# Performance work log

Hardware: AMD Instinct MI355X
Metric: run time of the kernel (lower is better)

Reference implementation:

```python
import jax, jax.numpy as jnp
import numpy as np

T, B = 128, 256
C_IN, H = 1024, 1024


def setup_inputs() -> dict:
    key = jax.random.key(0)
    ks = jax.random.split(key, 6)
    x = jax.random.normal(ks[0], (T * B, C_IN), dtype=jnp.float32)
    Wi = jax.random.normal(ks[1], (C_IN, 4 * H), dtype=jnp.float32) / np.sqrt(C_IN)
    Wh = jax.random.normal(ks[2], (H, 4 * H), dtype=jnp.float32) / np.sqrt(H)
    b = jax.random.normal(ks[3], (4 * H,), dtype=jnp.float32) * 0.01
    done = jax.random.randint(ks[4], (T * B,), 0, 2) > 0
    main = jax.random.randint(ks[5], (T * B,), 0, 2) > 0
    zeros = jnp.zeros((B, H), dtype=jnp.float32)
    return {"x": x, "c1": zeros, "h1": zeros, "c2": zeros, "h2": zeros,
            "Wi": Wi, "Wh": Wh, "b": b, "done": done, "main": main}


def reference(x, c1, h1, c2, h2, Wi, Wh, b, done, main):
    batch = c1.shape[0]
    num_steps = x.shape[0] // batch
    x3 = x.reshape(num_steps, batch, -1)
    done3 = done.reshape(num_steps, batch)
    main3 = main.reshape(num_steps, batch)

    def step(carry, inp):
        (r1c, r1h), (r2c, r2h) = carry
        xt, dt, mt = inp
        m = mt[:, None]  # [B,1] select player-1 vs player-2 state
        c = jnp.where(m, r1c, r2c)
        h = jnp.where(m, r1h, r2h)
        # OptimizedLSTMCell: fused gates, flax order i, f, g, o
        z = xt @ Wi + h @ Wh + b
        i, f, g, o = jnp.split(z, 4, axis=-1)
        nc = jax.nn.sigmoid(f) * c + jax.nn.sigmoid(i) * jnp.tanh(g)
        nh = jax.nn.sigmoid(o) * jnp.tanh(nc)
        # write back only to the active player's state
        n1c = jnp.where(m, nc, r1c); n1h = jnp.where(m, nh, r1h)
        n2c = jnp.where(m, r2c, nc); n2h = jnp.where(m, r2h, nh)
        # reset both states where episode is done
        d = dt[:, None]
        n1c = jnp.where(d, 0.0, n1c); n1h = jnp.where(d, 0.0, n1h)
        n2c = jnp.where(d, 0.0, n2c); n2h = jnp.where(d, 0.0, n2h)
        return ((n1c, n1h), (n2c, n2h)), nh

    _, ys = jax.lax.scan(step, ((c1, h1), (c2, h2)), (x3, done3, main3))
    return ys.reshape(-1, ys.shape[-1])  # [T*B, H]
```

## Files before the change

kernel.cpp:

```cpp
#include <hip/hip_runtime.h>
#include <cstdint>
#include <cstddef>

typedef unsigned short u16;
typedef unsigned char u8;
typedef unsigned int u32;

typedef short s16x8 __attribute__((ext_vector_type(8)));
typedef float f32x4 __attribute__((ext_vector_type(4)));

__device__ __forceinline__ float b2f(u16 h){ u32 u = ((u32)h)<<16; float f; __builtin_memcpy(&f,&u,4); return f; }
__device__ __forceinline__ u16 f2b(float x){ u32 u; __builtin_memcpy(&u,&x,4); u += 0x7fffu + ((u>>16)&1u); return (u16)(u>>16); }
__device__ __forceinline__ float sigf(float x){ return __builtin_amdgcn_rcpf(1.f+__expf(-x)); }
__device__ __forceinline__ float tanh2(float x){
  float ax=fabsf(x); float e=__expf(-2.f*ax);
  float r=(1.f-e)*__builtin_amdgcn_rcpf(1.f+e);
  return x<0.f? -r : r;
}

typedef __attribute__((address_space(1))) const void gvoid_t;
typedef __attribute__((address_space(3))) void lvoid_t;
__device__ __forceinline__ void gl_lds16(const u16* src, u16* dst){
  __builtin_amdgcn_global_load_lds((gvoid_t*)src, (lvoid_t*)dst, 16, 0, 0);
}

__device__ __forceinline__ s16x8 gload16_coh_s(const u16* sbase, u32 voff){
  s16x8 r;
  asm volatile("global_load_dwordx4 %0, %1, %2 sc0 sc1" : "=v"(r) : "v"(voff), "s"(sbase) : "memory");
  return r;
}
__device__ __forceinline__ float gloadf_s(const float* sbase, u32 voff){
  float r;
  asm volatile("global_load_dword %0, %1, %2" : "=v"(r) : "v"(voff), "s"(sbase) : "memory");
  return r;
}
__device__ __forceinline__ void st_u16_coh_s(u16* sbase, u32 voff, u16 v){
  asm volatile("global_store_short %0, %1, %2 sc0 sc1" :: "v"(voff), "v"((u32)v), "s"(sbase) : "memory");
}
__device__ __forceinline__ void st_f32_coh_s(float* sbase, u32 voff, float v){
  asm volatile("global_store_dword %0, %1, %2 sc0 sc1" :: "v"(voff), "v"(v), "s"(sbase) : "memory");
}
__device__ __forceinline__ s16x8 gload16(const u16* p){
  s16x8 r;
  asm volatile("global_load_dwordx4 %0, %1, off" : "=v"(r) : "v"(p) : "memory");
  return r;
}

__global__ void detect_mask_mode(const u8* raw, int n, int* flag){
  __shared__ int cnt;
  int tid = threadIdx.x;
  if(tid==0) cnt=0;
  __syncthreads();
  int c=0;
  for(int i=tid;i<n;i+=blockDim.x) c += (raw[i]!=0);
  atomicAdd(&cnt, c);
  __syncthreads();
  if(tid==0) *flag = (cnt > (n>>2)) ? 1 : 0;
}

__global__ void build_mcode(const void* done_raw, const void* main_raw, u8* code, int n, const int* flag){
  int mode = *flag;
  for(int i = blockIdx.x*blockDim.x + threadIdx.x; i<n; i += gridDim.x*blockDim.x){
    u8 d, m, m2;
    if(mode){
      d = ((const u8*)done_raw)[i]!=0; m = ((const u8*)main_raw)[i]!=0;
      m2 = (i+256<n) ? (((const u8*)main_raw)[i+256]!=0) : (u8)0;
    } else {
      d = ((const int*)done_raw)[i]!=0; m = ((const int*)main_raw)[i]!=0;
      m2 = (i+256<n) ? (((const int*)main_raw)[i+256]!=0) : (u8)0;
    }
    code[i] = d | (m<<1) | (m2<<2);
  }
}

__global__ void zero_flags(int* p, int n){
  int i = threadIdx.x;
  if(i<n) p[i]=0;
}

__global__ void cvt_f32_bf16(const float* __restrict__ in, u16* __restrict__ out, int n4){
  int i = blockIdx.x*blockDim.x + threadIdx.x;
  if(i < n4){
    float4 v = ((const float4*)in)[i];
    ushort4 o;
    o.x=f2b(v.x); o.y=f2b(v.y); o.z=f2b(v.z); o.w=f2b(v.w);
    ((ushort4*)out)[i]=o;
  }
}

__global__ void transpose_to_bf16(const float* __restrict__ in, u16* __restrict__ out, int R, int C){
  __shared__ float tile[64][65];
  int c0 = blockIdx.x*64, r0 = blockIdx.y*64;
  int tx = threadIdx.x & 63, ty = threadIdx.x >> 6;
  for(int i=ty;i<64;i+=4) tile[i][tx] = in[(size_t)(r0+i)*C + c0 + tx];
  __syncthreads();
  for(int i=ty;i<64;i+=4) out[(size_t)(c0+i)*R + r0 + tx] = f2b(tile[tx][i]);
}

__global__ void init_hsel(const float* __restrict__ h1in, const float* __restrict__ h2in,
                          const u8* __restrict__ mcode, u16* __restrict__ hsel0){
  int i = blockIdx.x*blockDim.x + threadIdx.x;
  if(i < 256*1024){
    int row = i >> 10;
    hsel0[i] = f2b((mcode[row]&2) ? h1in[i] : h2in[i]);
  }
}

template<bool ZF32>
__global__ __launch_bounds__(256) void gemm_zx(const u16* __restrict__ A, const u16* __restrict__ Bt,
                                               const float* __restrict__ bias, void* __restrict__ Cout,
                                               int M, int N, int K){
  __shared__ u16 As[128*32];
  __shared__ u16 Bs[128*32];
  int nbx = N>>7, nby = M>>7;
  int nwg = nbx*nby;
  int gid = blockIdx.x;
  int per = nwg>>3;
  int g2 = (gid&7)*per + (gid>>3);
  int tpg = 8*nbx;
  int grp = g2/tpg, w = g2%tpg;
  int brow = grp*8 + (w & 7);
  int bcol = w >> 3;
  int row0 = brow<<7, col0 = bcol<<7;

  int tid=threadIdx.x, wid=tid>>6, lane=tid&63;
  int l15=lane&15, hi=lane>>4;
  int wm=(wid>>1)<<6, wn=(wid&1)<<6;

  f32x4 acc[4][4];
  #pragma unroll
  for(int m=0;m<4;m++)
    #pragma unroll
    for(int n=0;n<4;n++) acc[m][n]=(f32x4){0.f,0.f,0.f,0.f};

  for(int k0=0;k0<K;k0+=32){
    __syncthreads();
    #pragma unroll
    for(int q=0;q<2;q++){
      int cb=q*256+wid*64;
      int ch=cb+lane;
      gl_lds16(A + (size_t)(row0+(ch>>2))*K + k0 + (ch&3)*8, &As[cb*8]);
    }
    #pragma unroll
    for(int q=0;q<2;q++){
      int cb=q*256+wid*64;
      int ch=cb+lane;
      gl_lds16(Bt + (size_t)(col0+(ch>>2))*K + k0 + (ch&3)*8, &Bs[cb*8]);
    }
    __syncthreads();
    s16x8 a[4], b[4];
    #pragma unroll
    for(int m=0;m<4;m++) a[m] = *(const s16x8*)&As[(wm+m*16+l15)*32 + hi*8];
    #pragma unroll
    for(int n=0;n<4;n++) b[n] = *(const s16x8*)&Bs[(wn+n*16+l15)*32 + hi*8];
    #pragma unroll
    for(int m=0;m<4;m++)
      #pragma unroll
      for(int n=0;n<4;n++)
        acc[m][n] = __builtin_amdgcn_mfma_f32_16x16x32_bf16(a[m],b[n],acc[m][n],0,0,0);
  }
  #pragma unroll
  for(int m=0;m<4;m++){
    #pragma unroll
    for(int n=0;n<4;n++){
      #pragma unroll
      for(int j=0;j<4;j++){
        int r = row0+wm+m*16+hi*4+j;
        int c = col0+wn+n*16+l15;
        float v = acc[m][n][j] + bias[c];
        if(ZF32) ((float*)Cout)[(size_t)r*N+c]=v;
        else     ((u16*)Cout)[(size_t)r*N+c]=f2b(v);
      }
    }
  }
}

template<bool ZF32>
__global__ __launch_bounds__(512) __attribute__((amdgpu_waves_per_eu(2,2)))
void lstm_persist(
    const void* __restrict__ Zx, const u16* __restrict__ Wht,
    u16* __restrict__ hs0, u16* __restrict__ hs1,
    const float* __restrict__ c1i, const float* __restrict__ h1i,
    const float* __restrict__ c2i, const float* __restrict__ h2i,
    const u8* __restrict__ mcode,
    float* __restrict__ out, int* __restrict__ ready)
{
  __shared__ u16 As[32768];
  __shared__ float zpart[4*2*32*33];
  __shared__ int lcnt[2];

  const int bid = blockIdx.x;
  const int rg = bid & 7, jg = bid >> 3;
  const int r0 = rg << 5, j0 = jg << 5;
  const int tid = threadIdx.x, wid = tid >> 6, lane = tid & 63;
  const int l15 = lane & 15, hi = lane >> 4;
  const int gate = wid >> 1, kg = wid & 1;
  const int srow = tid >> 4, sc16 = tid & 15;
  const int erow = tid >> 5, ecol = tid & 31;

  if(tid < 2) lcnt[tid] = 0;

  s16x8 breg[2][16];
  {
    #pragma unroll
    for(int n=0;n<2;n++){
      const u16* wp = Wht + ((size_t)(gate*1024 + j0 + n*16 + l15))*1024 + kg*512 + hi*8;
      #pragma unroll
      for(int kk=0;kk<16;kk++) breg[n][kk] = gload16(wp + kk*32);
    }
    asm volatile("s_waitcnt vmcnt(0)" ::: "memory");
    __builtin_amdgcn_sched_barrier(0);
  }

  float c1r[2],c2r[2],h1r[2],h2r[2];
  #pragma unroll
  for(int e=0;e<2;e++){
    size_t sidx = (size_t)(r0 + e*16 + erow)*1024 + j0 + ecol;
    c1r[e]=c1i[sidx]; c2r[e]=c2i[sidx]; h1r[e]=h1i[sidx]; h2r[e]=h2i[sidx];
  }

  u32 voffS[8];
  #pragma unroll
  for(int kc=0;kc<8;kc++) voffS[kc] = (u32)(((r0+srow)*1024 + (kc*16+sc16)*8)*2);
  u32 voffH[2], voffO[2];
  #pragma unroll
  for(int e=0;e<2;e++){
    u32 idx = (u32)((r0 + e*16 + erow)*1024 + j0 + ecol);
    voffH[e] = idx*2;
    voffO[e] = idx*4;
  }
  u32 voffZ[8];
  #pragma unroll
  for(int g=0;g<4;g++)
    #pragma unroll
    for(int e=0;e<2;e++)
      voffZ[g*2+e] = (u32)((((r0 + e*16 + erow)*4096) + g*1024 + j0 + ecol)*4);

  u16* pS = &As[sc16*256 + ((srow ^ (sc16&7))<<3)];
  const u16* pAe = &As[kg*16384 + hi*256 + ((l15 ^  hi   )<<3)];
  const u16* pAo = &As[kg*16384 + hi*256 + ((l15 ^ (4+hi))<<3)];
  float* pzw = &zpart[((gate*2+kg)*32 + hi*4)*33 + l15];
  const float* pzr = &zpart[erow*33 + ecol];

  const char* zstep = (const char*)Zx;
  const u16* Zb16 = (const u16*)Zx;
  float* outp = out;
  const u8* mp = mcode + r0;
  int* flag = ready + rg*32;

  #pragma unroll 1
  for(int t=0;t<128;t++){
    float zr[4][2];
    if(ZF32){
      #pragma unroll
      for(int g=0;g<4;g++)
        #pragma unroll
        for(int e=0;e<2;e++)
          zr[g][e] = gloadf_s((const float*)zstep, voffZ[g*2+e]);
    } else {
      #pragma unroll
      for(int g=0;g<4;g++)
        #pragma unroll
        for(int e=0;e<2;e++)
          zr[g][e] = b2f(Zb16[(size_t)(t*256 + r0 + e*16 + erow)*4096 + g*1024 + j0 + ecol]);
    }
    u8 cd0 = mp[erow], cd1 = mp[16+erow];

    if(t>0 && tid==0){
      while(__hip_atomic_load(flag, __ATOMIC_RELAXED, __HIP_MEMORY_SCOPE_AGENT) < 32*t)
        __builtin_amdgcn_s_sleep(1);
    }
    __syncthreads();
    __builtin_amdgcn_sched_barrier(0);

    const u16* hinp = (t&1) ? hs1 : hs0;
    u16* houtp = (t&1) ? hs0 : hs1;

    {
      s16x8 hv[8];
      #pragma unroll
      for(int kc=0;kc<8;kc++) hv[kc] = gload16_coh_s(hinp, voffS[kc]);
      asm volatile("s_waitcnt vmcnt(0)" ::: "memory");
      #pragma unroll
      for(int kc=0;kc<8;kc++) *(s16x8*)(pS + kc*4096) = hv[kc];
    }
    __syncthreads();

    f32x4 acc[2][2];
    #pragma unroll
    for(int m=0;m<2;m++)
      #pragma unroll
      for(int n=0;n<2;n++) acc[m][n]=(f32x4){0.f,0.f,0.f,0.f};
    #pragma unroll
    for(int kk=0;kk<16;kk++){
      const u16* p = (kk&1) ? pAo : pAe;
      s16x8 a0 = *(const s16x8*)(p + kk*1024);
      s16x8 a1 = *(const s16x8*)(p + kk*1024 + 128);
      acc[0][0] = __builtin_amdgcn_mfma_f32_16x16x32_bf16(a0, breg[0][kk], acc[0][0], 0,0,0);
      acc[0][1] = __builtin_amdgcn_mfma_f32_16x16x32_bf16(a0, breg[1][kk], acc[0][1], 0,0,0);
      acc[1][0] = __builtin_amdgcn_mfma_f32_16x16x32_bf16(a1, breg[0][kk], acc[1][0], 0,0,0);
      acc[1][1] = __builtin_amdgcn_mfma_f32_16x16x32_bf16(a1, breg[1][kk], acc[1][1], 0,0,0);
    }

    #pragma unroll
    for(int m=0;m<2;m++)
      #pragma unroll
      for(int n=0;n<2;n++)
        #pragma unroll
        for(int j=0;j<4;j++)
          pzw[m*528 + j*33 + n*16] = acc[m][n][j];
    __syncthreads();

    float nhv[2];
    #pragma unroll
    for(int e=0;e<2;e++){
      u8 cd = e ? cd1 : cd0;
      float zi  = zr[0][e] + pzr[0*1056 + e*528] + pzr[1*1056 + e*528];
      float zf_ = zr[1][e] + pzr[2*1056 + e*528] + pzr[3*1056 + e*528];
      float zg  = zr[2][e] + pzr[4*1056 + e*528] + pzr[5*1056 + e*528];
      float zo  = zr[3][e] + pzr[6*1056 + e*528] + pzr[7*1056 + e*528];
      bool d_ = cd & 1, m_ = cd & 2, m2 = cd & 4;
      float co = m_ ? c1r[e] : c2r[e];
      float nc = sigf(zf_)*co + sigf(zi)*tanh2(zg);
      float nhx = sigf(zo)*tanh2(nc);
      nhv[e] = nhx;
      float n1c = m_?nc:c1r[e], n2c = m_?c2r[e]:nc;
      float n1h = m_?nhx:h1r[e], n2h = m_?h2r[e]:nhx;
      if(d_){ n1c=0.f; n2c=0.f; n1h=0.f; n2h=0.f; }
      c1r[e]=n1c; c2r[e]=n2c; h1r[e]=n1h; h2r[e]=n2h;
      if(t<127)
        st_u16_coh_s(houtp, voffH[e], f2b(m2 ? n1h : n2h));
    }

    if(t<127){
      asm volatile("s_waitcnt vmcnt(0)" ::: "memory");
      if(lane==0){
        int c = atomicAdd(&lcnt[t&1], 1);
        if(c==7){
          lcnt[t&1] = 0;
          __hip_atomic_fetch_add(flag, 1, __ATOMIC_RELAXED, __HIP_MEMORY_SCOPE_AGENT);
        }
      }
    }

    #pragma unroll
    for(int e=0;e<2;e++)
      st_f32_coh_s(outp, voffO[e], nhv[e]);

    zstep += 4194304;
    outp  += 262144;
    mp    += 256;
  }
}

extern "C" void kernel_launch(void* const* d_in, const int* in_sizes, int n_in,
                              void* d_out, int out_size, void* d_ws, size_t ws_size,
                              hipStream_t stream){
  const float* x   = (const float*)d_in[0];
  const float* c1i = (const float*)d_in[1];
  const float* h1i = (const float*)d_in[2];
  const float* c2i = (const float*)d_in[3];
  const float* h2i = (const float*)d_in[4];
  const float* Wi  = (const float*)d_in[5];
  const float* Wh  = (const float*)d_in[6];
  const float* bias= (const float*)d_in[7];
  const void* done_raw = d_in[8];
  const void* main_raw = d_in[9];
  float* out = (float*)d_out;

  char* ws = (char*)d_ws;
  size_t off=0;
  auto alloc=[&](size_t sz)->char*{ char* p = ws+off; off += (sz+255)&~(size_t)255; return p; };

  u16* xb   = (u16*)alloc(33554432ull*2);
  u16* WiT  = (u16*)alloc(4096ull*1024*2);
  u16* WhT  = (u16*)alloc(4096ull*1024*2);
  u16* hs0  = (u16*)alloc(262144ull*2);
  u16* hs1  = (u16*)alloc(262144ull*2);
  u8* mcode = (u8*)alloc(32768);
  int* flag = (int*)alloc(256);
  int* ready= (int*)alloc(1024);

  bool zf32 = (off + 536870912ull) <= ws_size;
  void* Zx  = (void*)alloc(zf32 ? 536870912ull : 268435456ull);

  detect_mask_mode<<<1,256,0,stream>>>((const u8*)done_raw, 32768, flag);
  build_mcode<<<64,256,0,stream>>>(done_raw, main_raw, mcode, 32768, flag);
  cvt_f32_bf16<<<32768,256,0,stream>>>(x, xb, 8388608);
  transpose_to_bf16<<<dim3(64,16),256,0,stream>>>(Wi, WiT, 1024, 4096);
  transpose_to_bf16<<<dim3(64,16),256,0,stream>>>(Wh, WhT, 1024, 4096);
  init_hsel<<<1024,256,0,stream>>>(h1i, h2i, mcode, hs0);
  zero_flags<<<1,256,0,stream>>>(ready, 256);

  if(zf32) gemm_zx<true ><<<8192,256,0,stream>>>(xb, WiT, bias, Zx, 32768, 4096, 1024);
  else     gemm_zx<false><<<8192,256,0,stream>>>(xb, WiT, bias, Zx, 32768, 4096, 1024);

  if(zf32)
    lstm_persist<true ><<<256,512,0,stream>>>(Zx,WhT,hs0,hs1,c1i,h1i,c2i,h2i,mcode,out,ready);
  else
    lstm_persist<false><<<256,512,0,stream>>>(Zx,WhT,hs0,hs1,c1i,h1i,c2i,h2i,mcode,out,ready);
}
```

Measured before the change: 1.289 ms.

## Fuse input projection GEMM into persistent LSTM kernel, overlapped with step barrier

Removes the separate x@Wi GEMM kernel and its large Zx intermediate buffer. Each persistent block now computes its slice of x_t@Wi for the next step (bias folded into the accumulator init) right after publishing h, so this work overlaps with waiting on other blocks. The Wi slice is streamed from global memory or L2 every step, the block-to-(row, column) mapping is changed, and zpart now aliases the As LDS buffer, which needs an extra barrier. It also replaces the per-wave LDS counter signalling with one block-wide barrier and a single atomic per step.

```diff
diff --git a/kernel.cpp b/kernel.cpp
--- a/kernel.cpp
+++ b/kernel.cpp
@@ -8,6 +8,8 @@
 
 typedef short s16x8 __attribute__((ext_vector_type(8)));
 typedef float f32x4 __attribute__((ext_vector_type(4)));
+
+#define MF(a,b,c) __builtin_amdgcn_mfma_f32_16x16x32_bf16((a),(b),(c),0,0,0)
 
 __device__ __forceinline__ float b2f(u16 h){ u32 u = ((u32)h)<<16; float f; __builtin_memcpy(&f,&u,4); return f; }
 __device__ __forceinline__ u16 f2b(float x){ u32 u; __builtin_memcpy(&u,&x,4); u += 0x7fffu + ((u>>16)&1u); return (u16)(u>>16); }
@@ -18,31 +20,17 @@
   return x<0.f? -r : r;
 }
 
-typedef __attribute__((address_space(1))) const void gvoid_t;
-typedef __attribute__((address_space(3))) void lvoid_t;
-__device__ __forceinline__ void gl_lds16(const u16* src, u16* dst){
-  __builtin_amdgcn_global_load_lds((gvoid_t*)src, (lvoid_t*)dst, 16, 0, 0);
-}
-
-__device__ __forceinline__ s16x8 gload16_coh_s(const u16* sbase, u32 voff){
-  s16x8 r;
-  asm volatile("global_load_dwordx4 %0, %1, %2 sc0 sc1" : "=v"(r) : "v"(voff), "s"(sbase) : "memory");
-  return r;
-}
-__device__ __forceinline__ float gloadf_s(const float* sbase, u32 voff){
-  float r;
-  asm volatile("global_load_dword %0, %1, %2" : "=v"(r) : "v"(voff), "s"(sbase) : "memory");
-  return r;
-}
-__device__ __forceinline__ void st_u16_coh_s(u16* sbase, u32 voff, u16 v){
-  asm volatile("global_store_short %0, %1, %2 sc0 sc1" :: "v"(voff), "v"((u32)v), "s"(sbase) : "memory");
-}
-__device__ __forceinline__ void st_f32_coh_s(float* sbase, u32 voff, float v){
-  asm volatile("global_store_dword %0, %1, %2 sc0 sc1" :: "v"(voff), "v"(v), "s"(sbase) : "memory");
+__device__ __forceinline__ void st_u16_coh(u16* p, u16 v){
+  asm volatile("global_store_short %0, %1, off sc0 sc1" :: "v"(p), "v"((u32)v) : "memory");
 }
 __device__ __forceinline__ s16x8 gload16(const u16* p){
   s16x8 r;
   asm volatile("global_load_dwordx4 %0, %1, off" : "=v"(r) : "v"(p) : "memory");
+  return r;
+}
+__device__ __forceinline__ s16x8 gload16_coh(const u16* p){
+  s16x8 r;
+  asm volatile("global_load_dwordx4 %0, %1, off sc0 sc1" : "=v"(r) : "v"(p) : "memory");
   return r;
 }
 
@@ -106,91 +94,21 @@
   }
 }
 
-template<bool ZF32>
-__global__ __launch_bounds__(256) void gemm_zx(const u16* __restrict__ A, const u16* __restrict__ Bt,
-                                               const float* __restrict__ bias, void* __restrict__ Cout,
-                                               int M, int N, int K){
-  __shared__ u16 As[128*32];
-  __shared__ u16 Bs[128*32];
-  int nbx = N>>7, nby = M>>7;
-  int nwg = nbx*nby;
-  int gid = blockIdx.x;
-  int per = nwg>>3;
-  int g2 = (gid&7)*per + (gid>>3);
-  int tpg = 8*nbx;
-  int grp = g2/tpg, w = g2%tpg;
-  int brow = grp*8 + (w & 7);
-  int bcol = w >> 3;
-  int row0 = brow<<7, col0 = bcol<<7;
-
-  int tid=threadIdx.x, wid=tid>>6, lane=tid&63;
-  int l15=lane&15, hi=lane>>4;
-  int wm=(wid>>1)<<6, wn=(wid&1)<<6;
-
-  f32x4 acc[4][4];
-  #pragma unroll
-  for(int m=0;m<4;m++)
-    #pragma unroll
-    for(int n=0;n<4;n++) acc[m][n]=(f32x4){0.f,0.f,0.f,0.f};
-
-  for(int k0=0;k0<K;k0+=32){
-    __syncthreads();
-    #pragma unroll
-    for(int q=0;q<2;q++){
-      int cb=q*256+wid*64;
-      int ch=cb+lane;
-      gl_lds16(A + (size_t)(row0+(ch>>2))*K + k0 + (ch&3)*8, &As[cb*8]);
-    }
-    #pragma unroll
-    for(int q=0;q<2;q++){
-      int cb=q*256+wid*64;
-      int ch=cb+lane;
-      gl_lds16(Bt + (size_t)(col0+(ch>>2))*K + k0 + (ch&3)*8, &Bs[cb*8]);
-    }
-    __syncthreads();
-    s16x8 a[4], b[4];
-    #pragma unroll
-    for(int m=0;m<4;m++) a[m] = *(const s16x8*)&As[(wm+m*16+l15)*32 + hi*8];
-    #pragma unroll
-    for(int n=0;n<4;n++) b[n] = *(const s16x8*)&Bs[(wn+n*16+l15)*32 + hi*8];
-    #pragma unroll
-    for(int m=0;m<4;m++)
-      #pragma unroll
-      for(int n=0;n<4;n++)
-        acc[m][n] = __builtin_amdgcn_mfma_f32_16x16x32_bf16(a[m],b[n],acc[m][n],0,0,0);
-  }
-  #pragma unroll
-  for(int m=0;m<4;m++){
-    #pragma unroll
-    for(int n=0;n<4;n++){
-      #pragma unroll
-      for(int j=0;j<4;j++){
-        int r = row0+wm+m*16+hi*4+j;
-        int c = col0+wn+n*16+l15;
-        float v = acc[m][n][j] + bias[c];
-        if(ZF32) ((float*)Cout)[(size_t)r*N+c]=v;
-        else     ((u16*)Cout)[(size_t)r*N+c]=f2b(v);
-      }
-    }
-  }
-}
-
-template<bool ZF32>
 __global__ __launch_bounds__(512) __attribute__((amdgpu_waves_per_eu(2,2)))
-void lstm_persist(
-    const void* __restrict__ Zx, const u16* __restrict__ Wht,
+void lstm_fused(
+    const u16* __restrict__ xb, const u16* __restrict__ WiT,
+    const u16* __restrict__ Wht, const float* __restrict__ bias,
     u16* __restrict__ hs0, u16* __restrict__ hs1,
     const float* __restrict__ c1i, const float* __restrict__ h1i,
     const float* __restrict__ c2i, const float* __restrict__ h2i,
-    const u8* __restrict__ mcode,
-    float* __restrict__ out, int* __restrict__ ready)
+    const u8* __restrict__ mcode, float* __restrict__ out,
+    int* __restrict__ ready)
 {
   __shared__ u16 As[32768];
-  __shared__ float zpart[4*2*32*33];
-  __shared__ int lcnt[2];
+  float* zpart = (float*)As;
 
   const int bid = blockIdx.x;
-  const int rg = bid & 7, jg = bid >> 3;
+  const int rg = bid >> 5, jg = bid & 31;
   const int r0 = rg << 5, j0 = jg << 5;
   const int tid = threadIdx.x, wid = tid >> 6, lane = tid & 63;
   const int l15 = lane & 15, hi = lane >> 4;
@@ -198,8 +116,6 @@
   const int srow = tid >> 4, sc16 = tid & 15;
   const int erow = tid >> 5, ecol = tid & 31;
 
-  if(tid < 2) lcnt[tid] = 0;
-
   s16x8 breg[2][16];
   {
     #pragma unroll
@@ -211,6 +127,11 @@
     asm volatile("s_waitcnt vmcnt(0)" ::: "memory");
     __builtin_amdgcn_sched_barrier(0);
   }
+
+  const u16* wip0 = WiT + ((size_t)(gate*1024 + j0      + l15))*1024 + kg*512 + hi*8;
+  const u16* wip1 = WiT + ((size_t)(gate*1024 + j0 + 16 + l15))*1024 + kg*512 + hi*8;
+  const float bias0 = kg ? 0.f : bias[gate*1024 + j0      + l15];
+  const float bias1 = kg ? 0.f : bias[gate*1024 + j0 + 16 + l15];
 
   float c1r[2],c2r[2],h1r[2],h2r[2];
   #pragma unroll
@@ -219,52 +140,60 @@
     c1r[e]=c1i[sidx]; c2r[e]=c2i[sidx]; h1r[e]=h1i[sidx]; h2r[e]=h2i[sidx];
   }
 
-  u32 voffS[8];
-  #pragma unroll
-  for(int kc=0;kc<8;kc++) voffS[kc] = (u32)(((r0+srow)*1024 + (kc*16+sc16)*8)*2);
-  u32 voffH[2], voffO[2];
-  #pragma unroll
-  for(int e=0;e<2;e++){
-    u32 idx = (u32)((r0 + e*16 + erow)*1024 + j0 + ecol);
-    voffH[e] = idx*2;
-    voffO[e] = idx*4;
-  }
-  u32 voffZ[8];
-  #pragma unroll
-  for(int g=0;g<4;g++)
-    #pragma unroll
-    for(int e=0;e<2;e++)
-      voffZ[g*2+e] = (u32)((((r0 + e*16 + erow)*4096) + g*1024 + j0 + ecol)*4);
-
-  u16* pS = &As[sc16*256 + ((srow ^ (sc16&7))<<3)];
+  u16* pSh = &As[sc16*256 + ((srow ^ (sc16&7))<<3)];
   const u16* pAe = &As[kg*16384 + hi*256 + ((l15 ^  hi   )<<3)];
   const u16* pAo = &As[kg*16384 + hi*256 + ((l15 ^ (4+hi))<<3)];
   float* pzw = &zpart[((gate*2+kg)*32 + hi*4)*33 + l15];
   const float* pzr = &zpart[erow*33 + ecol];
 
-  const char* zstep = (const char*)Zx;
-  const u16* Zb16 = (const u16*)Zx;
-  float* outp = out;
-  const u8* mp = mcode + r0;
   int* flag = ready + rg*32;
 
-  #pragma unroll 1
+  f32x4 acc00, acc01, acc10, acc11;
+
+  auto xphase = [&](const u16* xrow){
+    s16x8 x0 = *(const s16x8*)(xrow + (0*16+sc16)*8);
+    s16x8 x1 = *(const s16x8*)(xrow + (1*16+sc16)*8);
+    s16x8 x2 = *(const s16x8*)(xrow + (2*16+sc16)*8);
+    s16x8 x3 = *(const s16x8*)(xrow + (3*16+sc16)*8);
+    s16x8 x4 = *(const s16x8*)(xrow + (4*16+sc16)*8);
+    s16x8 x5 = *(const s16x8*)(xrow + (5*16+sc16)*8);
+    s16x8 x6 = *(const s16x8*)(xrow + (6*16+sc16)*8);
+    s16x8 x7 = *(const s16x8*)(xrow + (7*16+sc16)*8);
+    *(s16x8*)(pSh + 0*4096) = x0;  *(s16x8*)(pSh + 1*4096) = x1;
+    *(s16x8*)(pSh + 2*4096) = x2;  *(s16x8*)(pSh + 3*4096) = x3;
+    *(s16x8*)(pSh + 4*4096) = x4;  *(s16x8*)(pSh + 5*4096) = x5;
+    *(s16x8*)(pSh + 6*4096) = x6;  *(s16x8*)(pSh + 7*4096) = x7;
+    __syncthreads();
+    acc00 = (f32x4){bias0,bias0,bias0,bias0};
+    acc01 = (f32x4){bias1,bias1,bias1,bias1};
+    acc10 = acc00; acc11 = acc01;
+    #pragma unroll
+    for(int g=0;g<4;g++){
+      s16x8 w0[4], w1[4];
+      #pragma unroll
+      for(int j=0;j<4;j++){
+        w0[j] = *(const s16x8*)(wip0 + (g*4+j)*32);
+        w1[j] = *(const s16x8*)(wip1 + (g*4+j)*32);
+      }
+      #pragma unroll
+      for(int j=0;j<4;j++){
+        int kk = g*4+j;
+        const u16* p = (kk&1) ? pAo : pAe;
+        s16x8 a0 = *(const s16x8*)(p + kk*1024);
+        s16x8 a1 = *(const s16x8*)(p + kk*1024 + 128);
+        acc00 = MF(a0, w0[j], acc00);
+        acc01 = MF(a0, w1[j], acc01);
+        acc10 = MF(a1, w0[j], acc10);
+        acc11 = MF(a1, w1[j], acc11);
+      }
+    }
+  };
+
+  xphase(xb + (size_t)(r0+srow)*1024);
+
   for(int t=0;t<128;t++){
-    float zr[4][2];
-    if(ZF32){
-      #pragma unroll
-      for(int g=0;g<4;g++)
-        #pragma unroll
-        for(int e=0;e<2;e++)
-          zr[g][e] = gloadf_s((const float*)zstep, voffZ[g*2+e]);
-    } else {
-      #pragma unroll
-      for(int g=0;g<4;g++)
-        #pragma unroll
-        for(int e=0;e<2;e++)
-          zr[g][e] = b2f(Zb16[(size_t)(t*256 + r0 + e*16 + erow)*4096 + g*1024 + j0 + ecol]);
-    }
-    u8 cd0 = mp[erow], cd1 = mp[16+erow];
+    u8 cd0 = mcode[t*256 + r0 + erow];
+    u8 cd1 = mcode[t*256 + r0 + 16 + erow];
 
     if(t>0 && tid==0){
       while(__hip_atomic_load(flag, __ATOMIC_RELAXED, __HIP_MEMORY_SCOPE_AGENT) < 32*t)
@@ -277,48 +206,52 @@
     u16* houtp = (t&1) ? hs0 : hs1;
 
     {
-      s16x8 hv[8];
-      #pragma unroll
-      for(int kc=0;kc<8;kc++) hv[kc] = gload16_coh_s(hinp, voffS[kc]);
+      const u16* hrow = hinp + (size_t)(r0+srow)*1024;
+      s16x8 h0 = gload16_coh(hrow + (0*16+sc16)*8);
+      s16x8 h1 = gload16_coh(hrow + (1*16+sc16)*8);
+      s16x8 h2 = gload16_coh(hrow + (2*16+sc16)*8);
+      s16x8 h3 = gload16_coh(hrow + (3*16+sc16)*8);
+      s16x8 h4 = gload16_coh(hrow + (4*16+sc16)*8);
+      s16x8 h5 = gload16_coh(hrow + (5*16+sc16)*8);
+      s16x8 h6 = gload16_coh(hrow + (6*16+sc16)*8);
+      s16x8 h7 = gload16_coh(hrow + (7*16+sc16)*8);
       asm volatile("s_waitcnt vmcnt(0)" ::: "memory");
-      #pragma unroll
-      for(int kc=0;kc<8;kc++) *(s16x8*)(pS + kc*4096) = hv[kc];
-    }
-    __syncthreads();
-
-    f32x4 acc[2][2];
-    #pragma unroll
-    for(int m=0;m<2;m++)
-      #pragma unroll
-      for(int n=0;n<2;n++) acc[m][n]=(f32x4){0.f,0.f,0.f,0.f};
+      *(s16x8*)(pSh + 0*4096) = h0;  *(s16x8*)(pSh + 1*4096) = h1;
+      *(s16x8*)(pSh + 2*4096) = h2;  *(s16x8*)(pSh + 3*4096) = h3;
+      *(s16x8*)(pSh + 4*4096) = h4;  *(s16x8*)(pSh + 5*4096) = h5;
+      *(s16x8*)(pSh + 6*4096) = h6;  *(s16x8*)(pSh + 7*4096) = h7;
+    }
+    __syncthreads();
+
     #pragma unroll
     for(int kk=0;kk<16;kk++){
       const u16* p = (kk&1) ? pAo : pAe;
       s16x8 a0 = *(const s16x8*)(p + kk*1024);
       s16x8 a1 = *(const s16x8*)(p + kk*1024 + 128);
-      acc[0][0] = __builtin_amdgcn_mfma_f32_16x16x32_bf16(a0, breg[0][kk], acc[0][0], 0,0,0);
-      acc[0][1] = __builtin_amdgcn_mfma_f32_16x16x32_bf16(a0, breg[1][kk], acc[0][1], 0,0,0);
-      acc[1][0] = __builtin_amdgcn_mfma_f32_16x16x32_bf16(a1, breg[0][kk], acc[1][0], 0,0,0);
-      acc[1][1] = __builtin_amdgcn_mfma_f32_16x16x32_bf16(a1, breg[1][kk], acc[1][1], 0,0,0);
-    }
-
-    #pragma unroll
-    for(int m=0;m<2;m++)
-      #pragma unroll
-      for(int n=0;n<2;n++)
-        #pragma unroll
-        for(int j=0;j<4;j++)
-          pzw[m*528 + j*33 + n*16] = acc[m][n][j];
+      acc00 = MF(a0, breg[0][kk], acc00);
+      acc01 = MF(a0, breg[1][kk], acc01);
+      acc10 = MF(a1, breg[0][kk], acc10);
+      acc11 = MF(a1, breg[1][kk], acc11);
+    }
+    __syncthreads();
+
+    #pragma unroll
+    for(int j=0;j<4;j++){
+      pzw[      j*33     ] = acc00[j];
+      pzw[      j*33 + 16] = acc01[j];
+      pzw[528 + j*33     ] = acc10[j];
+      pzw[528 + j*33 + 16] = acc11[j];
+    }
     __syncthreads();
 
     float nhv[2];
     #pragma unroll
     for(int e=0;e<2;e++){
       u8 cd = e ? cd1 : cd0;
-      float zi  = zr[0][e] + pzr[0*1056 + e*528] + pzr[1*1056 + e*528];
-      float zf_ = zr[1][e] + pzr[2*1056 + e*528] + pzr[3*1056 + e*528];
-      float zg  = zr[2][e] + pzr[4*1056 + e*528] + pzr[5*1056 + e*528];
-      float zo  = zr[3][e] + pzr[6*1056 + e*528] + pzr[7*1056 + e*528];
+      float zi  = pzr[   0 + e*528] + pzr[1056 + e*528];
+      float zf_ = pzr[2112 + e*528] + pzr[3168 + e*528];
+      float zg  = pzr[4224 + e*528] + pzr[5280 + e*528];
+      float zo  = pzr[6336 + e*528] + pzr[7392 + e*528];
       bool d_ = cd & 1, m_ = cd & 2, m2 = cd & 4;
       float co = m_ ? c1r[e] : c2r[e];
       float nc = sigf(zf_)*co + sigf(zi)*tanh2(zg);
@@ -328,28 +261,18 @@
       float n1h = m_?nhx:h1r[e], n2h = m_?h2r[e]:nhx;
       if(d_){ n1c=0.f; n2c=0.f; n1h=0.f; n2h=0.f; }
       c1r[e]=n1c; c2r[e]=n2c; h1r[e]=n1h; h2r[e]=n2h;
+      int grow = r0 + e*16 + erow;
       if(t<127)
-        st_u16_coh_s(houtp, voffH[e], f2b(m2 ? n1h : n2h));
-    }
-
-    if(t<127){
-      asm volatile("s_waitcnt vmcnt(0)" ::: "memory");
-      if(lane==0){
-        int c = atomicAdd(&lcnt[t&1], 1);
-        if(c==7){
-          lcnt[t&1] = 0;
-          __hip_atomic_fetch_add(flag, 1, __ATOMIC_RELAXED, __HIP_MEMORY_SCOPE_AGENT);
-        }
-      }
-    }
-
-    #pragma unroll
-    for(int e=0;e<2;e++)
-      st_f32_coh_s(outp, voffO[e], nhv[e]);
-
-    zstep += 4194304;
-    outp  += 262144;
-    mp    += 256;
+        st_u16_coh(&houtp[(size_t)grow*1024 + j0 + ecol], f2b(m2 ? n1h : n2h));
+      out[(size_t)(t*256 + grow)*1024 + j0 + ecol] = nhv[e];
+    }
+    asm volatile("s_waitcnt vmcnt(0)" ::: "memory");
+    __syncthreads();
+    if(t<127 && tid==0)
+      __hip_atomic_fetch_add(flag, 1, __ATOMIC_RELAXED, __HIP_MEMORY_SCOPE_AGENT);
+
+    if(t<127)
+      xphase(xb + (size_t)((t+1)*256 + r0 + srow)*1024);
   }
 }
 
@@ -380,9 +303,7 @@
   u8* mcode = (u8*)alloc(32768);
   int* flag = (int*)alloc(256);
   int* ready= (int*)alloc(1024);
-
-  bool zf32 = (off + 536870912ull) <= ws_size;
-  void* Zx  = (void*)alloc(zf32 ? 536870912ull : 268435456ull);
+  (void)ws_size;
 
   detect_mask_mode<<<1,256,0,stream>>>((const u8*)done_raw, 32768, flag);
   build_mcode<<<64,256,0,stream>>>(done_raw, main_raw, mcode, 32768, flag);
@@ -392,11 +313,6 @@
   init_hsel<<<1024,256,0,stream>>>(h1i, h2i, mcode, hs0);
   zero_flags<<<1,256,0,stream>>>(ready, 256);
 
-  if(zf32) gemm_zx<true ><<<8192,256,0,stream>>>(xb, WiT, bias, Zx, 32768, 4096, 1024);
-  else     gemm_zx<false><<<8192,256,0,stream>>>(xb, WiT, bias, Zx, 32768, 4096, 1024);
-
-  if(zf32)
-    lstm_persist<true ><<<256,512,0,stream>>>(Zx,WhT,hs0,hs1,c1i,h1i,c2i,h2i,mcode,out,ready);
-  else
-    lstm_persist<false><<<256,512,0,stream>>>(Zx,WhT,hs0,hs1,c1i,h1i,c2i,h2i,mcode,out,ready);
-}
+  lstm_fused<<<256,512,0,stream>>>(xb, WiT, WhT, bias, hs0, hs1,
+                                   c1i, h1i, c2i, h2i, mcode, out, ready);
+}
```

Measured after the change: 1.625 ms. 26.0% more time.
